# Kernel optimization log

Hardware: AMD Instinct MI355X
Metric: run time of the kernel (lower is better)

The kernel has to match this reference:

```python
import jax, jax.numpy as jnp
import numpy as np
import math

H = 2048          # hidden_size
NH = 16           # num_attn_heads
HD = H // NH      # attn head dim = 128
NFW = 4           # num_lact_heads
FD = H // NFW     # fw head dim = 512
DH = FD           # inter_multi = 1.0
CHUNK = 512       # lact_chunk_size
WINDOW = 2048     # window_size
ROPE_BASE = 500000.0
BASE_LR_INV = math.log(math.expm1(0.001))  # inv_softplus(1e-3)


def rmsnorm(x, w, eps=1e-6):
    return x * jax.lax.rsqrt(jnp.mean(x * x, axis=-1, keepdims=True) + eps) * w


def l2norm(x, eps=1e-12):
    return x * jax.lax.rsqrt(jnp.sum(x * x, axis=-1, keepdims=True) + eps)


def rope(x):  # x: [b, h, s, d], half-split convention
    d = x.shape[-1]
    s = x.shape[2]
    inv = 1.0 / (ROPE_BASE ** (jnp.arange(d // 2, dtype=jnp.float32) / (d // 2)))
    f = jnp.arange(s, dtype=jnp.float32)[:, None] * inv[None, :]  # [s, d/2]
    cos, sin = jnp.cos(f), jnp.sin(f)
    x1, x2 = x[..., : d // 2], x[..., d // 2:]
    return jnp.concatenate([x1 * cos - x2 * sin, x2 * cos + x1 * sin], axis=-1)


def setup_inputs() -> dict:
    key = jax.random.key(0)
    ks = jax.random.split(key, 8)
    b, s = 2, 2048
    return {
        "hidden_states": jax.random.normal(ks[0], (b, s, H), jnp.float32),
        "qkv_w": jax.random.normal(ks[1], (3 * H, H), jnp.float32) / math.sqrt(H),
        "q_norm_w": jnp.ones((H,), jnp.float32),
        "k_norm_w": jnp.ones((H,), jnp.float32),
        "qk_scale": jnp.ones((H, 2), jnp.float32),
        "qk_offset": jnp.zeros((H, 2), jnp.float32),
        "lr_w": jax.random.normal(ks[2], (3 * NFW, H), jnp.float32) / math.sqrt(H),
        "lr_b": jnp.zeros((3 * NFW,), jnp.float32),
        "w0": jax.random.normal(ks[3], (NFW, DH, FD), jnp.float32) / math.sqrt(FD),
        "w1": jax.random.normal(ks[4], (NFW, FD, DH), jnp.float32) / math.sqrt(DH),
        "w2": jax.random.normal(ks[5], (NFW, DH, FD), jnp.float32) / math.sqrt(FD),
        "ttt_norm_w": jnp.ones((FD,), jnp.float32),
        "o_proj_w": jax.random.normal(ks[6], (H, H), jnp.float32) / math.sqrt(H),
    }


def reference(hidden_states, qkv_w, q_norm_w, k_norm_w, qk_scale, qk_offset,
              lr_w, lr_b, w0, w1, w2, ttt_norm_w, o_proj_w):
    x = hidden_states
    b, s, _ = x.shape
    nc = s // CHUNK

    qkv = x @ qkv_w.T
    q, k, v = jnp.split(qkv, 3, axis=-1)
    q = rmsnorm(q, q_norm_w)
    k = rmsnorm(k, k_norm_w)

    # ---- TTT (fast-weight SwiGLU) branch ----
    fq = jax.nn.silu(q * qk_scale[:, 0] + qk_offset[:, 0])
    fk = jax.nn.silu(k * qk_scale[:, 1] + qk_offset[:, 1])
    fv = jax.nn.silu(v)
    tohead = lambda t: t.reshape(b, s, NFW, FD).transpose(0, 2, 1, 3)  # [b,h,s,d]
    fq, fk, fv = l2norm(tohead(fq)), l2norm(tohead(fk)), tohead(fv)

    lr = jax.nn.softplus(x @ lr_w.T + lr_b + BASE_LR_INV)          # [b,s,3*NFW]
    lr = lr.reshape(b, s, 3, NFW).transpose(2, 0, 3, 1)[..., None]  # [3,b,h,s,1]
    lr0, lr1, lr2 = lr[0], lr[1], lr[2]

    chunkify = lambda t: t.reshape(b, NFW, nc, CHUNK, -1).transpose(2, 0, 1, 3, 4)
    qs, ks_, vs = chunkify(fq), chunkify(fk), chunkify(fv)
    l0s, l1s, l2s = chunkify(lr0), chunkify(lr1), chunkify(lr2)

    w0b = jnp.broadcast_to(w0, (b,) + w0.shape)
    w1b = jnp.broadcast_to(w1, (b,) + w1.shape)
    w2b = jnp.broadcast_to(w2, (b,) + w2.shape)

    def step(carry, xs):
        w0c, w1c, w2c = carry
        qc, kc, vc, l0, l1, l2 = xs
        # apply current fast weights to queries (strictly causal across chunks)
        hq = jax.nn.silu(jnp.einsum('bhcd,bhed->bhce', qc, w0c)) * \
             jnp.einsum('bhcd,bhed->bhce', qc, w2c)
        oc = jnp.einsum('bhce,bhde->bhcd', hq, w1c)
        # gradient-descent update on dot-product loss -sum(v * f(k))
        g1 = jnp.einsum('bhcd,bhed->bhce', kc, w0c)
        g2 = jnp.einsum('bhcd,bhed->bhce', kc, w2c)
        gate = jax.nn.silu(g1)
        hidden = gate * g2
        dhidden = jnp.einsum('bhcd,bhde->bhce', vc, w1c)  # w1^T v
        dh2 = dhidden * gate
        sig = jax.nn.sigmoid(g1)
        dh1 = dhidden * g2 * (sig * (1.0 + g1 * (1.0 - sig)))  # silu'(g1)
        w1n = w1c + jnp.einsum('bhcd,bhce->bhde', l1 * vc, hidden)
        w0n = w0c + jnp.einsum('bhce,bhcd->bhed', l0 * dh1, kc)
        w2n = w2c + jnp.einsum('bhce,bhcd->bhed', l2 * dh2, kc)
        return (w0n, w1n, w2n), oc

    _, o_chunks = jax.lax.scan(step, (w0b, w1b, w2b), (qs, ks_, vs, l0s, l1s, l2s))
    o_ttt = o_chunks.transpose(1, 2, 0, 3, 4).reshape(b, NFW, s, FD)
    o_ttt = rmsnorm(o_ttt, ttt_norm_w)
    o_ttt = o_ttt.transpose(0, 2, 1, 3).reshape(b, s, H)

    # ---- sliding-window attention branch ----
    qa = rope(q.reshape(b, s, NH, HD).transpose(0, 2, 1, 3))
    ka = rope(k.reshape(b, s, NH, HD).transpose(0, 2, 1, 3))
    va = v.reshape(b, s, NH, HD).transpose(0, 2, 1, 3)
    scores = jnp.einsum('bhqd,bhkd->bhqk', qa, ka) / math.sqrt(HD)
    i = jnp.arange(s)
    mask = (i[:, None] >= i[None, :]) & (i[:, None] - i[None, :] < WINDOW)
    scores = jnp.where(mask, scores, jnp.float32(-1e9))
    p = jax.nn.softmax(scores, axis=-1)
    attn = jnp.einsum('bhqk,bhkd->bhqd', p, va).transpose(0, 2, 1, 3).reshape(b, s, H)

    return (attn + o_ttt) @ o_proj_w.T
```

## Files before the change

kernel.cpp:

```cpp
#include <hip/hip_runtime.h>
#include <hip/hip_bf16.h>
#include <math.h>

using bf16 = __hip_bfloat16;

namespace {

constexpr int cH = 2048;
constexpr int cNH = 16;
constexpr int cHD = 128;
constexpr int cNFW = 4;
constexpr int cFD = 512;
constexpr int cS = 2048;
constexpr float cRSQRT_HD = 0.08838834764831845f;
constexpr long ZL_ = 262144;
constexpr long ZG_ = 1048576;

typedef __attribute__((ext_vector_type(8))) short short8;
typedef __attribute__((ext_vector_type(4))) float f32x4;

__device__ __forceinline__ float sigmoidf_(float x) { return 1.0f / (1.0f + __expf(-x)); }
__device__ __forceinline__ float b2f(bf16 v) { return __bfloat162float(v); }
__device__ __forceinline__ bf16 f2b(float v) { return __float2bfloat16(v); }
__device__ __forceinline__ unsigned short f2bu(float f) {
  return __builtin_bit_cast(unsigned short, __float2bfloat16(f));
}
__device__ __forceinline__ float bu2f(unsigned u) { return __uint_as_float(u << 16); }

#if defined(__has_builtin)
#if __has_builtin(__builtin_amdgcn_global_load_lds)
#define HAVE_GLOAD 1
#endif
#endif

__device__ __forceinline__ void gload16(const bf16* g, short* ldsbase) {
#ifdef HAVE_GLOAD
  __builtin_amdgcn_global_load_lds((const __attribute__((address_space(1))) void*)g,
                                   (__attribute__((address_space(3))) void*)ldsbase, 16, 0, 0);
#else
  const int l = threadIdx.x & 63;
  *(uint4*)(ldsbase + l * 8) = *(const uint4*)g;
#endif
}

__device__ __forceinline__ void stage16(const bf16* src, short* dst) {
  *(uint4*)dst = *(const uint4*)src;
  *(uint4*)(dst + 8) = *(const uint4*)(src + 8);
}

__device__ __forceinline__ void store1(float* p, float v) { *p = v; }
__device__ __forceinline__ void store1(bf16* p, float v) { *p = f2b(v); }

__device__ __forceinline__ void mm_core32(const bf16* __restrict__ Ab, int lda,
                                          const bf16* __restrict__ Bb, int ldb, int K,
                                          short* As, short* Bs, f32x4 acc[4][4]) {
  const int t = threadIdx.x, lane = t & 63, g = lane >> 4, c16 = lane & 15;
  const int wv = t >> 6, wm = (wv >> 1) * 64, wn = (wv & 1) * 64;
  for (int k0 = 0; k0 < K; k0 += 32) {
    __syncthreads();
    {
      const int ch = wv * 2;
      const bf16* ga = Ab + (size_t)(ch * 16 + (lane >> 2)) * lda + k0 + (lane & 3) * 8;
      gload16(ga, &As[ch * 512]);
      gload16(ga + (size_t)16 * lda, &As[ch * 512 + 512]);
      const bf16* gb = Bb + (size_t)(ch * 16 + (lane >> 2)) * ldb + k0 + (lane & 3) * 8;
      gload16(gb, &Bs[ch * 512]);
      gload16(gb + (size_t)16 * ldb, &Bs[ch * 512 + 512]);
    }
    __syncthreads();
    short8 af[4], bfr[4];
#pragma unroll
    for (int mi = 0; mi < 4; ++mi) af[mi] = *(const short8*)&As[(wm + mi * 16 + c16) * 32 + g * 8];
#pragma unroll
    for (int ni = 0; ni < 4; ++ni) bfr[ni] = *(const short8*)&Bs[(wn + ni * 16 + c16) * 32 + g * 8];
#pragma unroll
    for (int mi = 0; mi < 4; ++mi)
#pragma unroll
      for (int ni = 0; ni < 4; ++ni)
        acc[mi][ni] = __builtin_amdgcn_mfma_f32_16x16x32_bf16(af[mi], bfr[ni], acc[mi][ni], 0, 0, 0);
  }
}

template <bool ACC, bool MIR, typename TC>
__device__ __forceinline__ void mm_store(TC* Cb, bf16* Mb, int ldc, int rb, int cb, f32x4 acc[4][4]) {
  const int t = threadIdx.x, lane = t & 63, g = lane >> 4, c16 = lane & 15;
  const int wv = t >> 6, wm = (wv >> 1) * 64, wn = (wv & 1) * 64;
  const int rbase = rb + wm, cbase = cb + wn;
#pragma unroll
  for (int mi = 0; mi < 4; ++mi)
#pragma unroll
    for (int ni = 0; ni < 4; ++ni) {
      const int col = cbase + ni * 16 + c16;
#pragma unroll
      for (int r = 0; r < 4; ++r) {
        const int row = rbase + mi * 16 + g * 4 + r;
        TC* cp = Cb + (size_t)row * ldc + col;
        if constexpr (ACC) {
          float nv = *cp + acc[mi][ni][r];
          *cp = nv;
          if constexpr (MIR) Mb[(size_t)row * ldc + col] = f2b(nv);
        } else {
          store1(cp, acc[mi][ni][r]);
        }
      }
    }
}

template <typename TC>
__global__ __launch_bounds__(512, 1) void k_mm8(const bf16* __restrict__ A, int lda,
                                                const bf16* __restrict__ B, int ldb,
                                                TC* __restrict__ C, int ldc, int K) {
  __shared__ short LA[3][256 * 64];
  __shared__ short LB[3][128 * 64];
  const int t = threadIdx.x, lane = t & 63, wv = t >> 6;
  const int g = lane >> 4, c16 = lane & 15;
  const int wm = (wv >> 1) * 64, wn = (wv & 1) * 64;
  const bf16* Ab = A + (size_t)blockIdx.y * 256 * lda;
  const bf16* Bb = B + (size_t)blockIdx.x * 128 * ldb;
  const int NKT = K >> 6;
  const int srow = wv * 16 + (lane >> 3);
  const int scol = ((lane & 7) ^ ((lane >> 3) & 7)) * 8;

  auto stA = [&](int buf, int half, int kt) {
    const int ktc = (kt < NKT) ? kt : 0;
    const bf16* src = Ab + (size_t)(half * 128 + srow) * lda + ktc * 64 + scol;
    short* dst = &LA[buf][(half * 128 + wv * 16) * 64];
    gload16(src, dst);
    gload16(src + (size_t)8 * lda, dst + 512);
  };
  auto stB = [&](int buf, int kt) {
    const int ktc = (kt < NKT) ? kt : 0;
    const bf16* src = Bb + (size_t)srow * ldb + ktc * 64 + scol;
    short* dst = &LB[buf][(wv * 16) * 64];
    gload16(src, dst);
    gload16(src + (size_t)8 * ldb, dst + 512);
  };

  f32x4 acc[4][4];
  const f32x4 zero4 = {0.f, 0.f, 0.f, 0.f};
#pragma unroll
  for (int i = 0; i < 4; ++i)
#pragma unroll
    for (int j = 0; j < 4; ++j) acc[i][j] = zero4;

  stA(0, 0, 0); stA(0, 1, 0); stB(0, 0);
  stA(1, 0, 1); stA(1, 1, 1); stB(1, 1);
  asm volatile("s_waitcnt vmcnt(6)" ::: "memory");
  __builtin_amdgcn_s_barrier();

  for (int kt = 0; kt < NKT; ++kt) {
    const int cb = kt % 3, nb = (kt + 2) % 3;
    short8 af[4][2], bfr[4][2];
#pragma unroll
    for (int f = 0; f < 4; ++f)
#pragma unroll
      for (int kk = 0; kk < 2; ++kk) {
        const int ra = wm + f * 16 + c16;
        af[f][kk] = *(const short8*)&LA[cb][ra * 64 + ((kk * 4 + g) ^ (ra & 7)) * 8];
        const int rb_ = wn + f * 16 + c16;
        bfr[f][kk] = *(const short8*)&LB[cb][rb_ * 64 + ((kk * 4 + g) ^ (rb_ & 7)) * 8];
      }
    stA(nb, 0, kt + 2); stA(nb, 1, kt + 2); stB(nb, kt + 2);
    __builtin_amdgcn_s_setprio(1);
#pragma unroll
    for (int f = 0; f < 4; ++f)
#pragma unroll
      for (int ni = 0; ni < 4; ++ni)
#pragma unroll
        for (int kk = 0; kk < 2; ++kk)
          acc[f][ni] = __builtin_amdgcn_mfma_f32_16x16x32_bf16(
              af[f][kk], bfr[ni][kk], acc[f][ni], 0, 0, 0);
    __builtin_amdgcn_s_setprio(0);
    asm volatile("s_waitcnt vmcnt(6)" ::: "memory");
    __builtin_amdgcn_s_barrier();
  }

  const int rbase = blockIdx.y * 256 + wm, cbase = blockIdx.x * 128 + wn;
#pragma unroll
  for (int fr = 0; fr < 4; ++fr)
#pragma unroll
    for (int ni = 0; ni < 4; ++ni) {
      const int col = cbase + ni * 16 + c16;
#pragma unroll
      for (int r = 0; r < 4; ++r)
        store1(C + (size_t)(rbase + fr * 16 + g * 4 + r) * ldc + col, acc[fr][ni][r]);
    }
}

__global__ __launch_bounds__(256) void k_fuse1(const bf16* __restrict__ fq, const bf16* __restrict__ fk,
                                               const bf16* __restrict__ fv,
                                               const bf16* __restrict__ w0b, const bf16* __restrict__ w1t,
                                               const bf16* __restrict__ w2b,
                                               bf16* __restrict__ hq, bf16* __restrict__ trH,
                                               bf16* __restrict__ trD1, bf16* __restrict__ trD2,
                                               bf16* __restrict__ trK, bf16* __restrict__ trV,
                                               const float* __restrict__ lr0, const float* __restrict__ lr1,
                                               const float* __restrict__ lr2,
                                               const bf16* __restrict__ occ,
                                               const float* __restrict__ tw, bf16* __restrict__ y,
                                               int chunk) {
  __shared__ short S[12288];
  __shared__ float red[4];
  const int id = blockIdx.x, t = threadIdx.x;
  const size_t choff = (size_t)chunk * 262144;

  if (id < 512) {
    const int bh = id >> 6, tile = id & 63, by = tile >> 3, bx = tile & 7;
    const int lane = t & 63, g = lane >> 4, c16 = lane & 15, wv = t >> 6;
    const int wm = (wv >> 1) * 32, wn = (wv & 1) * 32;
    const bf16* Aq = fq + (size_t)bh * ZG_ + choff + (size_t)(by * 64) * cFD;
    const bf16* Ak = fk + (size_t)bh * ZG_ + choff + (size_t)(by * 64) * cFD;
    const bf16* Av = fv + (size_t)bh * ZG_ + choff + (size_t)(by * 64) * cFD;
    const bf16* B0 = w0b + (size_t)bh * ZL_ + (size_t)(bx * 64) * cFD;
    const bf16* B2 = w2b + (size_t)bh * ZL_ + (size_t)(bx * 64) * cFD;
    const bf16* B1 = w1t + (size_t)bh * ZL_ + (size_t)(bx * 64) * cFD;

    f32x4 acc[5][2][2];
    const f32x4 zero4 = {0.f, 0.f, 0.f, 0.f};
#pragma unroll
    for (int v = 0; v < 5; ++v)
#pragma unroll
      for (int i = 0; i < 2; ++i)
#pragma unroll
        for (int j = 0; j < 2; ++j) acc[v][i][j] = zero4;

    const int srow = wv * 16 + (lane >> 2), scol = (lane & 3) * 8;
    for (int k0 = 0; k0 < 512; k0 += 32) {
      __syncthreads();
      gload16(Aq + (size_t)srow * cFD + k0 + scol, &S[0 + wv * 512]);
      gload16(Ak + (size_t)srow * cFD + k0 + scol, &S[2048 + wv * 512]);
      gload16(Av + (size_t)srow * cFD + k0 + scol, &S[4096 + wv * 512]);
      gload16(B0 + (size_t)srow * cFD + k0 + scol, &S[6144 + wv * 512]);
      gload16(B2 + (size_t)srow * cFD + k0 + scol, &S[8192 + wv * 512]);
      gload16(B1 + (size_t)srow * cFD + k0 + scol, &S[10240 + wv * 512]);
      __syncthreads();
      short8 aq[2], ak[2], av[2], b0[2], b2[2], b1[2];
#pragma unroll
      for (int mi = 0; mi < 2; ++mi) {
        const int ro = (wm + mi * 16 + c16) * 32 + g * 8;
        aq[mi] = *(const short8*)&S[0 + ro];
        ak[mi] = *(const short8*)&S[2048 + ro];
        av[mi] = *(const short8*)&S[4096 + ro];
      }
#pragma unroll
      for (int ni = 0; ni < 2; ++ni) {
        const int ro = (wn + ni * 16 + c16) * 32 + g * 8;
        b0[ni] = *(const short8*)&S[6144 + ro];
        b2[ni] = *(const short8*)&S[8192 + ro];
        b1[ni] = *(const short8*)&S[10240 + ro];
      }
#pragma unroll
      for (int mi = 0; mi < 2; ++mi)
#pragma unroll
        for (int ni = 0; ni < 2; ++ni) {
          acc[0][mi][ni] = __builtin_amdgcn_mfma_f32_16x16x32_bf16(aq[mi], b0[ni], acc[0][mi][ni], 0, 0, 0);
          acc[1][mi][ni] = __builtin_amdgcn_mfma_f32_16x16x32_bf16(aq[mi], b2[ni], acc[1][mi][ni], 0, 0, 0);
          acc[2][mi][ni] = __builtin_amdgcn_mfma_f32_16x16x32_bf16(ak[mi], b0[ni], acc[2][mi][ni], 0, 0, 0);
          acc[3][mi][ni] = __builtin_amdgcn_mfma_f32_16x16x32_bf16(ak[mi], b2[ni], acc[3][mi][ni], 0, 0, 0);
          acc[4][mi][ni] = __builtin_amdgcn_mfma_f32_16x16x32_bf16(av[mi], b1[ni], acc[4][mi][ni], 0, 0, 0);
        }
    }

    float l0v[2][4], l2v[2][4];
#pragma unroll
    for (int mi = 0; mi < 2; ++mi)
#pragma unroll
      for (int r = 0; r < 4; ++r) {
        const int row = by * 64 + wm + mi * 16 + g * 4 + r;
        l0v[mi][r] = lr0[bh * 2048 + chunk * 512 + row];
        l2v[mi][r] = lr2[bh * 2048 + chunk * 512 + row];
      }
#pragma unroll
    for (int mi = 0; mi < 2; ++mi)
#pragma unroll
      for (int ni = 0; ni < 2; ++ni)
#pragma unroll
        for (int r = 0; r < 4; ++r) {
          float hq1 = acc[0][mi][ni][r], hq2 = acc[1][mi][ni][r];
          float g1 = acc[2][mi][ni][r], g2 = acc[3][mi][ni][r], dh = acc[4][mi][ni][r];
          acc[0][mi][ni][r] = hq1 * sigmoidf_(hq1) * hq2;
          float sg = sigmoidf_(g1);
          float gate = g1 * sg;
          acc[1][mi][ni][r] = gate * g2;
          acc[2][mi][ni][r] = l0v[mi][r] * dh * g2 * (sg * (1.0f + g1 * (1.0f - sg)));
          acc[3][mi][ni][r] = l2v[mi][r] * dh * gate;
        }

    short* Ts = S;
    bf16* dst0 = hq + (size_t)bh * ZL_;
    bf16* dstT[3] = {trH + (size_t)bh * ZL_, trD1 + (size_t)bh * ZL_, trD2 + (size_t)bh * ZL_};
#pragma unroll
    for (int rd = 0; rd < 4; ++rd) {
      __syncthreads();
#pragma unroll
      for (int mi = 0; mi < 2; ++mi)
#pragma unroll
        for (int ni = 0; ni < 2; ++ni)
#pragma unroll
          for (int r = 0; r < 4; ++r) {
            const int row = wm + mi * 16 + g * 4 + r, col = wn + ni * 16 + c16;
            if (rd == 0) Ts[row * 66 + col] = (short)f2bu(acc[0][mi][ni][r]);
            else Ts[col * 66 + row] = (short)f2bu(acc[rd][mi][ni][r]);
          }
      __syncthreads();
      const int rr = t >> 2, cs = (t & 3) * 16;
      unsigned short u[16] __attribute__((aligned(16)));
#pragma unroll
      for (int i = 0; i < 16; ++i) u[i] = (unsigned short)Ts[rr * 66 + cs + i];
      bf16* dp = (rd == 0) ? (dst0 + (size_t)(by * 64 + rr) * cFD + bx * 64 + cs)
                           : (dstT[rd - 1] + (size_t)(bx * 64 + rr) * cFD + by * 64 + cs);
      *(uint4*)dp = *(uint4*)u;
      *(uint4*)(dp + 8) = *(uint4*)(u + 8);
    }
  } else if (id < 1536) {
    short* Ts = S;
    const int id2 = id - 512;
    const int var = id2 >> 9, bh = (id2 >> 6) & 7, by = (id2 >> 3) & 7, bx = id2 & 7;
    const bf16* src = ((var == 0) ? fk : fv) + choff + (size_t)bh * ZG_;
    bf16* dst = ((var == 0) ? trK : trV) + (size_t)bh * ZL_;
    {
      const int rr = t >> 2, cseg = (t & 3) * 16;
      if (var == 0) {
        stage16(src + (size_t)(by * 64 + rr) * cFD + bx * 64 + cseg, &Ts[rr * 72 + cseg]);
      } else {
        const float s = lr1[bh * 2048 + chunk * 512 + by * 64 + rr];
        const bf16* p = src + (size_t)(by * 64 + rr) * cFD + bx * 64 + cseg;
        unsigned short u[16] __attribute__((aligned(16)));
#pragma unroll
        for (int i = 0; i < 16; ++i) u[i] = f2bu(b2f(p[i]) * s);
        *(uint4*)&Ts[rr * 72 + cseg] = *(uint4*)u;
        *(uint4*)&Ts[rr * 72 + cseg + 8] = *(uint4*)(u + 8);
      }
    }
    __syncthreads();
    {
      const int oc_ = t >> 2, rseg = (t & 3) * 16;
      unsigned short u[16] __attribute__((aligned(16)));
#pragma unroll
      for (int i = 0; i < 16; ++i) u[i] = (unsigned short)Ts[(rseg + i) * 72 + oc_];
      bf16* dp = dst + (size_t)(bx * 64 + oc_) * cFD + by * 64 + rseg;
      *(uint4*)dp = *(uint4*)u;
      *(uint4*)(dp + 8) = *(uint4*)(u + 8);
    }
  } else {
    const int rrow = id - 1536;
    const int bh = rrow >> 9, rr = rrow & 511;
    const bf16* src = occ + ((size_t)bh * 512 + rr) * 512;
    float v0 = b2f(src[t]), v1 = b2f(src[t + 256]);
    float ss = v0 * v0 + v1 * v1;
    for (int d = 32; d; d >>= 1) ss += __shfl_down(ss, d);
    if ((t & 63) == 0) red[t >> 6] = ss;
    __syncthreads();
    const float rstd = rsqrtf((red[0] + red[1] + red[2] + red[3]) / cFD + 1e-6f);
    const int si = (chunk - 1) * 512 + rr;
    bf16* dst = y + ((size_t)((bh >> 2) * cS) + si) * cH + (bh & 3) * cFD;
    dst[t] = f2b(b2f(dst[t]) + v0 * rstd * tw[t]);
    dst[t + 256] = f2b(b2f(dst[t + 256]) + v1 * rstd * tw[t + 256]);
  }
}

__global__ __launch_bounds__(256) void k_updna(const bf16* __restrict__ trV, const bf16* __restrict__ trH,
                                               const bf16* __restrict__ trD1, const bf16* __restrict__ trD2,
                                               const bf16* __restrict__ trK,
                                               const bf16* __restrict__ hq, const bf16* __restrict__ w1bc,
                                               float* w0s, float* w1s, float* w2s,
                                               bf16* w0b, bf16* w1bn, bf16* w2b, bf16* w1t,
                                               bf16* __restrict__ occ) {
  __shared__ short Sh[8704];
  const int id = blockIdx.x, t = threadIdx.x;
  const int lane = t & 63, g = lane >> 4, c16 = lane & 15, wv = t >> 6;
  if (id < 384) {
    short* As = Sh;
    short* Bs = Sh + 4096;
    const int z = id >> 4, tile = id & 15, by = tile >> 2, bx = tile & 3;
    const int var = z >> 3, bh = z & 7;
    const bf16 *Aa, *Bb;
    if (var == 0) {
      Aa = trV + (size_t)bh * ZL_ + (size_t)by * 128 * cFD;
      Bb = trH + (size_t)bh * ZL_ + (size_t)bx * 128 * cFD;
    } else if (var == 1) {
      Aa = trD1 + (size_t)bh * ZL_ + (size_t)by * 128 * cFD;
      Bb = trK + (size_t)bh * ZL_ + (size_t)bx * 128 * cFD;
    } else {
      Aa = trD2 + (size_t)bh * ZL_ + (size_t)by * 128 * cFD;
      Bb = trK + (size_t)bh * ZL_ + (size_t)bx * 128 * cFD;
    }
    f32x4 acc[4][4];
    const f32x4 zero4 = {0.f, 0.f, 0.f, 0.f};
#pragma unroll
    for (int i = 0; i < 4; ++i)
#pragma unroll
      for (int j = 0; j < 4; ++j) acc[i][j] = zero4;
    mm_core32(Aa, cFD, Bb, cFD, cFD, As, Bs, acc);
    if (var == 1) {
      mm_store<true, true>(w0s + (size_t)bh * ZL_, w0b + (size_t)bh * ZL_, cFD, by * 128, bx * 128, acc);
    } else if (var == 2) {
      mm_store<true, true>(w2s + (size_t)bh * ZL_, w2b + (size_t)bh * ZL_, cFD, by * 128, bx * 128, acc);
    } else {
      float* W = w1s + (size_t)bh * ZL_;
      bf16* M = w1bn + (size_t)bh * ZL_;
      const int wm = (wv >> 1) * 64, wn = (wv & 1) * 64;
#pragma unroll
      for (int mi = 0; mi < 4; ++mi)
#pragma unroll
        for (int ni = 0; ni < 4; ++ni) {
          const int col = bx * 128 + wn + ni * 16 + c16;
#pragma unroll
          for (int r = 0; r < 4; ++r) {
            const int row = by * 128 + wm + mi * 16 + g * 4 + r;
            float nv = W[(size_t)row * cFD + col] + acc[mi][ni][r];
            W[(size_t)row * cFD + col] = nv;
            M[(size_t)row * cFD + col] = f2b(nv);
            acc[mi][ni][r] = nv;
          }
        }
      bf16* T = w1t + (size_t)bh * ZL_;
      short* Ts = Sh;
#pragma unroll
      for (int rd = 0; rd < 2; ++rd) {
        __syncthreads();
        if (wn == rd * 64) {
#pragma unroll
          for (int mi = 0; mi < 4; ++mi)
#pragma unroll
            for (int ni = 0; ni < 4; ++ni) {
              const int cc = ni * 16 + c16;
              unsigned short u[4] __attribute__((aligned(8)));
#pragma unroll
              for (int r = 0; r < 4; ++r) u[r] = f2bu(acc[mi][ni][r]);
              *(uint2*)&Ts[cc * 136 + wm + mi * 16 + g * 4] = *(uint2*)u;
            }
        }
        __syncthreads();
        const int cc = t >> 2, seg = (t & 3) * 32;
        unsigned short u[32] __attribute__((aligned(16)));
#pragma unroll
        for (int i = 0; i < 32; ++i) u[i] = (unsigned short)Ts[cc * 136 + seg + i];
        bf16* dp = T + (size_t)(bx * 128 + rd * 64 + cc) * cFD + by * 128 + seg;
        *(uint4*)dp = *(uint4*)u;
        *(uint4*)(dp + 8) = *(uint4*)(u + 8);
        *(uint4*)(dp + 16) = *(uint4*)(u + 16);
        *(uint4*)(dp + 24) = *(uint4*)(u + 24);
      }
    }
  } else {
    short* As = Sh;
    short* Bs = Sh + 4096;
    const int id2 = id - 384;
    const int bh = id2 >> 4, tile = id2 & 15, by = tile >> 2, bx = tile & 3;
    const bf16* Aa = hq + (size_t)bh * ZL_ + (size_t)by * 128 * cFD;
    const bf16* Bb = w1bc + (size_t)bh * ZL_ + (size_t)bx * 128 * cFD;
    f32x4 acc[4][4];
    const f32x4 zero4 = {0.f, 0.f, 0.f, 0.f};
#pragma unroll
    for (int i = 0; i < 4; ++i)
#pragma unroll
      for (int j = 0; j < 4; ++j) acc[i][j] = zero4;
    mm_core32(Aa, cFD, Bb, cFD, cFD, As, Bs, acc);
    mm_store<false, false>(occ + (size_t)bh * ZL_, (bf16*)nullptr, cFD, by * 128, bx * 128, acc);
  }
}

__global__ __launch_bounds__(256) void k_normcvt(const bf16* __restrict__ occ,
                                                 const float* __restrict__ tw, bf16* __restrict__ y,
                                                 const float* __restrict__ opw, bf16* __restrict__ opwb,
                                                 int chunk) {
  __shared__ float red[4];
  const int id = blockIdx.x, t = threadIdx.x;
  if (id < 4096) {
    const int bh = id >> 9, rr = id & 511;
    const bf16* src = occ + ((size_t)bh * 512 + rr) * 512;
    float v0 = b2f(src[t]), v1 = b2f(src[t + 256]);
    float ss = v0 * v0 + v1 * v1;
    for (int d = 32; d; d >>= 1) ss += __shfl_down(ss, d);
    if ((t & 63) == 0) red[t >> 6] = ss;
    __syncthreads();
    const float rstd = rsqrtf((red[0] + red[1] + red[2] + red[3]) / cFD + 1e-6f);
    const int si = chunk * 512 + rr;
    bf16* dst = y + ((size_t)((bh >> 2) * cS) + si) * cH + (bh & 3) * cFD;
    dst[t] = f2b(b2f(dst[t]) + v0 * rstd * tw[t]);
    dst[t + 256] = f2b(b2f(dst[t + 256]) + v1 * rstd * tw[t + 256]);
  } else {
    const size_t i = ((size_t)(id - 4096) * 256 + t) * 8;
    float4 a = *(const float4*)(opw + i), b = *(const float4*)(opw + i + 4);
    unsigned short u[8] __attribute__((aligned(16)));
    u[0] = f2bu(a.x); u[1] = f2bu(a.y); u[2] = f2bu(a.z); u[3] = f2bu(a.w);
    u[4] = f2bu(b.x); u[5] = f2bu(b.y); u[6] = f2bu(b.z); u[7] = f2bu(b.w);
    *(uint4*)(opwb + i) = *(uint4*)u;
  }
}

__global__ __launch_bounds__(256) void k_prep(const float* __restrict__ x, const float* __restrict__ qkv_w,
                                              const float* __restrict__ w0, const float* __restrict__ w1,
                                              const float* __restrict__ w2,
                                              const float* __restrict__ lr_w, const float* __restrict__ lr_b,
                                              bf16* __restrict__ xb, bf16* __restrict__ qkvwb,
                                              float* __restrict__ w0s, float* __restrict__ w1s,
                                              float* __restrict__ w2s,
                                              float* __restrict__ ct, float* __restrict__ stb,
                                              float* lr0, float* lr1, float* lr2, float base) {
  __shared__ float xbuf[cH];
  const int id = blockIdx.x, t = threadIdx.x;
  if (id < 4096) {
    const size_t i = ((size_t)id * 256 + t) * 8;
    float4 a = *(const float4*)(x + i), b = *(const float4*)(x + i + 4);
    unsigned short u[8] __attribute__((aligned(16)));
    u[0] = f2bu(a.x); u[1] = f2bu(a.y); u[2] = f2bu(a.z); u[3] = f2bu(a.w);
    u[4] = f2bu(b.x); u[5] = f2bu(b.y); u[6] = f2bu(b.z); u[7] = f2bu(b.w);
    *(uint4*)(xb + i) = *(uint4*)u;
  } else if (id < 10240) {
    const size_t i = ((size_t)(id - 4096) * 256 + t) * 8;
    float4 a = *(const float4*)(qkv_w + i), b = *(const float4*)(qkv_w + i + 4);
    unsigned short u[8] __attribute__((aligned(16)));
    u[0] = f2bu(a.x); u[1] = f2bu(a.y); u[2] = f2bu(a.z); u[3] = f2bu(a.w);
    u[4] = f2bu(b.x); u[5] = f2bu(b.y); u[6] = f2bu(b.z); u[7] = f2bu(b.w);
    *(uint4*)(qkvwb + i) = *(uint4*)u;
  } else if (id < 16384) {
    const int sub = id - 10240;
    const int w = sub >> 11, blk = sub & 2047;
    const size_t i = ((size_t)blk * 256 + t) * 4;
    const int f = (int)((i >> 18) & 3);
    const size_t off = i & 262143;
    const float* src = (w == 0) ? w0 : (w == 1) ? w1 : w2;
    float* dst = (w == 0) ? w0s : (w == 1) ? w1s : w2s;
    *(float4*)(dst + i) = *(const float4*)(src + (size_t)f * 262144 + off);
  } else if (id < 16896) {
    const int gid = (id - 16384) * 256 + t;
    const int si = gid >> 6, jj = gid & 63;
    float inv = powf(500000.0f, -(float)jj / 64.0f);
    float ang = (float)si * inv;
    ct[(size_t)si * 64 + jj] = cosf(ang);
    stb[(size_t)si * 64 + jj] = sinf(ang);
  } else {
    const int token = id - 16896, b_ = token >> 11, si = token & 2047;
    const int wv = t >> 6, lane = t & 63;
    const float* xr = x + (size_t)token * cH;
    for (int i = t; i < cH; i += 256) xbuf[i] = xr[i];
    __syncthreads();
#pragma unroll
    for (int jj = 0; jj < 3; ++jj) {
      const int j = wv * 3 + jj;
      const float* wr = lr_w + (size_t)j * cH;
      float s = 0.f;
      for (int k = lane; k < cH; k += 64) s += xbuf[k] * wr[k];
      for (int d = 32; d; d >>= 1) s += __shfl_down(s, d);
      if (lane == 0) {
        float v = s + lr_b[j] + base;
        float sp = (v > 15.f) ? v : log1pf(expf(v));
        const int tt = j >> 2, f = j & 3;
        float* dst = (tt == 0 ? lr0 : tt == 1 ? lr1 : lr2);
        dst[(size_t)(b_ * cNFW + f) * cS + si] = sp;
      }
    }
  }
}

__global__ __launch_bounds__(256) void k_post2(bf16* __restrict__ qkvh,
                                               const float* __restrict__ qnw, const float* __restrict__ knw,
                                               const float* __restrict__ ct, const float* __restrict__ stb,
                                               bf16* __restrict__ qa, bf16* __restrict__ ka,
                                               bf16* __restrict__ vt) {
  __shared__ short smem[8704];
  __shared__ float red[4];
  const int id = blockIdx.x, t = threadIdx.x;
  if (id < 4096) {
    float* buf = (float*)smem;
    const int token = id, b_ = token >> 11, si = token & 2047;
    bf16* base = qkvh + (size_t)token * 3 * cH;
    for (int pass = 0; pass < 2; ++pass) {
      __syncthreads();
      bf16* src = base + pass * cH;
      const float* nw = pass ? knw : qnw;
      float ss = 0.f;
      for (int i = t; i < cH; i += 256) {
        float v = b2f(src[i]);
        buf[i] = v;
        ss += v * v;
      }
      for (int d = 32; d; d >>= 1) ss += __shfl_down(ss, d);
      if ((t & 63) == 0) red[t >> 6] = ss;
      __syncthreads();
      const float rstd = rsqrtf((red[0] + red[1] + red[2] + red[3]) / cH + 1e-6f);
      for (int i = t; i < cH; i += 256) {
        float v = buf[i] * rstd * nw[i];
        buf[i] = v;
        src[i] = f2b(v);
      }
      __syncthreads();
      bf16* dst = pass ? ka : qa;
      const float scale = pass ? 1.f : cRSQRT_HD;
      const int hh = t >> 4, j0 = (t & 15) * 4;
      const float* cr = ct + (size_t)si * 64 + j0;
      const float* sr = stb + (size_t)si * 64 + j0;
      bf16* drow = dst + ((size_t)(b_ * cNH + hh) * cS + si) * cHD;
      unsigned short u1[4] __attribute__((aligned(8))), u2[4] __attribute__((aligned(8)));
#pragma unroll
      for (int i = 0; i < 4; ++i) {
        float x1 = buf[hh * cHD + j0 + i], x2 = buf[hh * cHD + 64 + j0 + i];
        u1[i] = f2bu((x1 * cr[i] - x2 * sr[i]) * scale);
        u2[i] = f2bu((x2 * cr[i] + x1 * sr[i]) * scale);
      }
      *(uint2*)(drow + j0) = *(uint2*)u1;
      *(uint2*)(drow + 64 + j0) = *(uint2*)u2;
    }
  } else {
    short* Ts = smem;
    const int id2 = id - 4096;
    const int tile = id2 & 31, h = (id2 >> 5) & 15, b_ = id2 >> 9;
    {
      const int r = t >> 2, seg = (t & 3) * 32;
      const bf16* src = qkvh + ((size_t)(b_ * cS) + tile * 64 + r) * 3 * cH + 2 * cH + h * cHD + seg;
      stage16(src, &Ts[r * 136 + seg]);
      stage16(src + 16, &Ts[r * 136 + seg + 16]);
    }
    __syncthreads();
    {
      const int d = t >> 1, seg2 = (t & 1) * 32;
      unsigned short u[32] __attribute__((aligned(16)));
#pragma unroll
      for (int i = 0; i < 32; ++i) u[i] = (unsigned short)Ts[(seg2 + i) * 136 + d];
      bf16* dp = vt + ((size_t)(b_ * cNH + h) * cHD + d) * cS + tile * 64 + seg2;
      *(uint4*)dp = *(uint4*)u;
      *(uint4*)(dp + 8) = *(uint4*)(u + 8);
      *(uint4*)(dp + 16) = *(uint4*)(u + 16);
      *(uint4*)(dp + 24) = *(uint4*)(u + 24);
    }
  }
}

__global__ __launch_bounds__(256) void k_mid(const bf16* __restrict__ qkvh,
                                             const float* __restrict__ qk_scale,
                                             const float* __restrict__ qk_offset,
                                             bf16* fq, bf16* fk, bf16* fv,
                                             const float* __restrict__ w0s_, bf16* __restrict__ w0b_,
                                             const float* __restrict__ w1s_, bf16* __restrict__ w1t_) {
  __shared__ short Ts[64 * 72];
  const int id = blockIdx.x, t = threadIdx.x;
  if (id < 4096) {
    const int token = id, b_ = token >> 11, si = token & 2047;
    const bf16* base = qkvh + (size_t)token * 3 * cH;
#pragma unroll
    for (int pass = 0; pass < 2; ++pass) {
      const bf16* src = base + pass * cH;
      bf16* fdst = pass ? fk : fq;
      const int head = t >> 6, lane = t & 63;
      float f[8];
      float ss2 = 0.f;
#pragma unroll
      for (int k = 0; k < 8; ++k) {
        const int idx = head * cFD + lane + k * 64;
        float v = b2f(src[idx]);
        float u = v * qk_scale[idx * 2 + pass] + qk_offset[idx * 2 + pass];
        float fv_ = u * sigmoidf_(u);
        f[k] = fv_;
        ss2 += fv_ * fv_;
      }
      for (int d = 1; d < 64; d <<= 1) ss2 += __shfl_xor(ss2, d);
      const float sc2 = rsqrtf(ss2 + 1e-12f);
      bf16* dst = fdst + ((size_t)(b_ * cNFW + head) * cS + si) * cFD;
#pragma unroll
      for (int k = 0; k < 8; ++k) dst[lane + k * 64] = f2b(f[k] * sc2);
    }
    const bf16* vr = base + 2 * cH;
    for (int i = t; i < cH; i += 256) {
      float v = b2f(vr[i]);
      fv[((size_t)(b_ * cNFW + (i >> 9)) * cS + si) * cFD + (i & 511)] = f2b(v * sigmoidf_(v));
    }
  } else if (id < 7168) {
    const size_t i = ((size_t)(id - 4096) * 256 + t) * 8;
    float4 a = *(const float4*)(w0s_ + i), b = *(const float4*)(w0s_ + i + 4);
    unsigned short u[8] __attribute__((aligned(16)));
    u[0] = f2bu(a.x); u[1] = f2bu(a.y); u[2] = f2bu(a.z); u[3] = f2bu(a.w);
    u[4] = f2bu(b.x); u[5] = f2bu(b.y); u[6] = f2bu(b.z); u[7] = f2bu(b.w);
    *(uint4*)(w0b_ + i) = *(uint4*)u;
  } else {
    const int id3 = id - 7168;
    const int bh = id3 >> 6, tile = id3 & 63, by = tile >> 3, bx = tile & 7;
    {
      const int rr = t >> 2, cseg = (t & 3) * 16;
      const float* p = w1s_ + (size_t)bh * ZL_ + (size_t)(by * 64 + rr) * cFD + bx * 64 + cseg;
      unsigned short u[16] __attribute__((aligned(16)));
#pragma unroll
      for (int i = 0; i < 16; ++i) u[i] = f2bu(p[i]);
      *(uint4*)&Ts[rr * 72 + cseg] = *(uint4*)u;
      *(uint4*)&Ts[rr * 72 + cseg + 8] = *(uint4*)(u + 8);
    }
    __syncthreads();
    {
      const int oc_ = t >> 2, rseg = (t & 3) * 16;
      unsigned short u[16] __attribute__((aligned(16)));
#pragma unroll
      for (int i = 0; i < 16; ++i) u[i] = (unsigned short)Ts[(rseg + i) * 72 + oc_];
      bf16* dp = w1t_ + (size_t)bh * ZL_ + (size_t)(bx * 64 + oc_) * cFD + by * 64 + rseg;
      *(uint4*)dp = *(uint4*)u;
      *(uint4*)(dp + 8) = *(uint4*)(u + 8);
    }
  }
}

__global__ __launch_bounds__(512) void k_attn6(const bf16* __restrict__ qa, const bf16* __restrict__ ka,
                                               const bf16* __restrict__ vt, bf16* __restrict__ y) {
  const int id = blockIdx.x;
  const int xcd = id & 7;
  const int j = id >> 3;
  const int p = j & 7;
  const int hb = (j >> 3) * 8 + xcd;
  const int h = hb & 15, b_ = hb >> 4;
  __shared__ short KsP[9216];
  __shared__ short Vts[128 * 72];
  const int t = threadIdx.x, lane = t & 63, g = lane >> 4, c16 = lane & 15, wv = t >> 6;
  const size_t hbq = (size_t)(b_ * cNH + h) * cS;
  const bf16* vb = vt + (size_t)(b_ * cNH + h) * (size_t)(cHD * cS);
  const int r = t >> 3, seg = (t & 7) * 16;
  const int dv = t >> 2, seg2 = (t & 3) * 16;
  const f32x4 zero4 = {0.f, 0.f, 0.f, 0.f};

  for (int half = 0; half < 2; ++half) {
    const int qt = half ? p : 15 - p;
    const int q0 = qt * 128;
    const int nkt = 2 * qt + 2;
    short8 qf[4];
    {
      const bf16* qsrc = qa + (hbq + q0 + wv * 16 + c16) * cHD;
#pragma unroll
      for (int ks = 0; ks < 4; ++ks) qf[ks] = *(const short8*)(qsrc + ks * 32 + g * 8);
    }
    f32x4 o[8];
#pragma unroll
    for (int i = 0; i < 8; ++i) o[i] = zero4;
    float m[4], l[4];
#pragma unroll
    for (int rr = 0; rr < 4; ++rr) { m[rr] = -1e30f; l[rr] = 0.f; }

    uint4 kp0, kp1, vp0, vp1;
    {
      const bf16* ksrc = ka + (hbq + r) * cHD + seg;
      kp0 = *(const uint4*)ksrc; kp1 = *(const uint4*)(ksrc + 8);
      const bf16* vsrc = vb + (size_t)dv * cS + seg2;
      vp0 = *(const uint4*)vsrc; vp1 = *(const uint4*)(vsrc + 8);
    }

    for (int kt = 0; kt < nkt; ++kt) {
      __syncthreads();
      {
        short* kd = &KsP[r * 136 + seg];
        *(uint4*)kd = kp0; *(uint4*)(kd + 8) = kp1;
        short* vd = &Vts[dv * 72 + seg2];
        *(uint4*)vd = vp0; *(uint4*)(vd + 8) = vp1;
      }
      __syncthreads();
      if (kt + 1 < nkt) {
        const bf16* ksrc = ka + (hbq + (kt + 1) * 64 + r) * cHD + seg;
        kp0 = *(const uint4*)ksrc; kp1 = *(const uint4*)(ksrc + 8);
        const bf16* vsrc = vb + (size_t)dv * cS + (kt + 1) * 64 + seg2;
        vp0 = *(const uint4*)vsrc; vp1 = *(const uint4*)(vsrc + 8);
      } else if (half == 0) {
        const bf16* ksrc = ka + (hbq + r) * cHD + seg;
        kp0 = *(const uint4*)ksrc; kp1 = *(const uint4*)(ksrc + 8);
        const bf16* vsrc = vb + (size_t)dv * cS + seg2;
        vp0 = *(const uint4*)vsrc; vp1 = *(const uint4*)(vsrc + 8);
      }
// ... 179 lines not shown
```

Baseline: 660.8 us.

## Load GEMM A operand directly into registers, bypassing LDS staging

In the k_mm8 GEMM, the A tile is no longer staged through a triple-buffered LDS array. Each wave now reads its A fragments straight from global memory into registers, using an even/odd register double buffer. The main loop is unrolled by two so it can alternate between the two buffers. B keeps its LDS triple buffer. This drops the LDS traffic and footprint for A, but waves that share rows now fetch the same A data twice. The strided 16-byte per-lane global loads may also coalesce poorly, and the loop assumes an even K-tile count.

```diff
diff --git a/kernel.cpp b/kernel.cpp
--- a/kernel.cpp
+++ b/kernel.cpp
@@ -110,7 +110,6 @@
 __global__ __launch_bounds__(512, 1) void k_mm8(const bf16* __restrict__ A, int lda,
                                                 const bf16* __restrict__ B, int ldb,
                                                 TC* __restrict__ C, int ldc, int K) {
-  __shared__ short LA[3][256 * 64];
   __shared__ short LB[3][128 * 64];
   const int t = threadIdx.x, lane = t & 63, wv = t >> 6;
   const int g = lane >> 4, c16 = lane & 15;
@@ -121,13 +120,6 @@
   const int srow = wv * 16 + (lane >> 3);
   const int scol = ((lane & 7) ^ ((lane >> 3) & 7)) * 8;
 
-  auto stA = [&](int buf, int half, int kt) {
-    const int ktc = (kt < NKT) ? kt : 0;
-    const bf16* src = Ab + (size_t)(half * 128 + srow) * lda + ktc * 64 + scol;
-    short* dst = &LA[buf][(half * 128 + wv * 16) * 64];
-    gload16(src, dst);
-    gload16(src + (size_t)8 * lda, dst + 512);
-  };
   auto stB = [&](int buf, int kt) {
     const int ktc = (kt < NKT) ? kt : 0;
     const bf16* src = Bb + (size_t)srow * ldb + ktc * 64 + scol;
@@ -135,6 +127,15 @@
     gload16(src, dst);
     gload16(src + (size_t)8 * ldb, dst + 512);
   };
+  auto loadA = [&](short8 dst[4][2], int kt) {
+    const int ktc = (kt < NKT) ? kt : 0;
+#pragma unroll
+    for (int f = 0; f < 4; ++f)
+#pragma unroll
+      for (int kk = 0; kk < 2; ++kk)
+        dst[f][kk] = *(const short8*)(Ab + (size_t)(wm + f * 16 + c16) * lda +
+                                      ktc * 64 + kk * 32 + g * 8);
+  };
 
   f32x4 acc[4][4];
   const f32x4 zero4 = {0.f, 0.f, 0.f, 0.f};
@@ -143,36 +144,70 @@
 #pragma unroll
     for (int j = 0; j < 4; ++j) acc[i][j] = zero4;
 
-  stA(0, 0, 0); stA(0, 1, 0); stB(0, 0);
-  stA(1, 0, 1); stA(1, 1, 1); stB(1, 1);
-  asm volatile("s_waitcnt vmcnt(6)" ::: "memory");
+  short8 afE[4][2], afO[4][2];
+
+  stB(0, 0);
+  stB(1, 1);
+  loadA(afE, 0);
+  asm volatile("s_waitcnt vmcnt(0)" ::: "memory");
   __builtin_amdgcn_s_barrier();
 
-  for (int kt = 0; kt < NKT; ++kt) {
-    const int cb = kt % 3, nb = (kt + 2) % 3;
-    short8 af[4][2], bfr[4][2];
-#pragma unroll
-    for (int f = 0; f < 4; ++f)
-#pragma unroll
-      for (int kk = 0; kk < 2; ++kk) {
-        const int ra = wm + f * 16 + c16;
-        af[f][kk] = *(const short8*)&LA[cb][ra * 64 + ((kk * 4 + g) ^ (ra & 7)) * 8];
-        const int rb_ = wn + f * 16 + c16;
-        bfr[f][kk] = *(const short8*)&LB[cb][rb_ * 64 + ((kk * 4 + g) ^ (rb_ & 7)) * 8];
-      }
-    stA(nb, 0, kt + 2); stA(nb, 1, kt + 2); stB(nb, kt + 2);
-    __builtin_amdgcn_s_setprio(1);
-#pragma unroll
-    for (int f = 0; f < 4; ++f)
+  int rb = 0;
+  for (int it = 0; it < NKT; it += 2) {
+    {
+      const int kt = it;
+      const int sb = (rb >= 1) ? rb - 1 : 2;
+      loadA(afO, kt + 1);
+      stB(sb, kt + 2);
+      short8 bfr[4][2];
 #pragma unroll
       for (int ni = 0; ni < 4; ++ni)
 #pragma unroll
-        for (int kk = 0; kk < 2; ++kk)
-          acc[f][ni] = __builtin_amdgcn_mfma_f32_16x16x32_bf16(
-              af[f][kk], bfr[ni][kk], acc[f][ni], 0, 0, 0);
-    __builtin_amdgcn_s_setprio(0);
-    asm volatile("s_waitcnt vmcnt(6)" ::: "memory");
-    __builtin_amdgcn_s_barrier();
+        for (int kk = 0; kk < 2; ++kk) {
+          const int rr = wn + ni * 16 + c16;
+          bfr[ni][kk] = *(const short8*)&LB[rb][rr * 64 + ((kk * 4 + g) ^ (rr & 7)) * 8];
+        }
+      __builtin_amdgcn_s_setprio(1);
+#pragma unroll
+      for (int f = 0; f < 4; ++f)
+#pragma unroll
+        for (int ni = 0; ni < 4; ++ni)
+#pragma unroll
+          for (int kk = 0; kk < 2; ++kk)
+            acc[f][ni] = __builtin_amdgcn_mfma_f32_16x16x32_bf16(
+                afE[f][kk], bfr[ni][kk], acc[f][ni], 0, 0, 0);
+      __builtin_amdgcn_s_setprio(0);
+      asm volatile("s_waitcnt vmcnt(4)" ::: "memory");
+      __builtin_amdgcn_s_barrier();
+      rb = (rb + 1 < 3) ? rb + 1 : 0;
+    }
+    {
+      const int kt = it + 1;
+      const int sb = (rb >= 1) ? rb - 1 : 2;
+      loadA(afE, kt + 1);
+      stB(sb, kt + 2);
+      short8 bfr[4][2];
+#pragma unroll
+      for (int ni = 0; ni < 4; ++ni)
+#pragma unroll
+        for (int kk = 0; kk < 2; ++kk) {
+          const int rr = wn + ni * 16 + c16;
+          bfr[ni][kk] = *(const short8*)&LB[rb][rr * 64 + ((kk * 4 + g) ^ (rr & 7)) * 8];
+        }
+      __builtin_amdgcn_s_setprio(1);
+#pragma unroll
+      for (int f = 0; f < 4; ++f)
+#pragma unroll
+        for (int ni = 0; ni < 4; ++ni)
+#pragma unroll
+          for (int kk = 0; kk < 2; ++kk)
+            acc[f][ni] = __builtin_amdgcn_mfma_f32_16x16x32_bf16(
+                afO[f][kk], bfr[ni][kk], acc[f][ni], 0, 0, 0);
+      __builtin_amdgcn_s_setprio(0);
+      asm volatile("s_waitcnt vmcnt(4)" ::: "memory");
+      __builtin_amdgcn_s_barrier();
+      rb = (rb + 1 < 3) ? rb + 1 : 0;
+    }
   }
 
   const int rbase = blockIdx.y * 256 + wm, cbase = blockIdx.x * 128 + wn;
```

Result: slower. 819.1 us (+24.0%).

## Triple-buffer LDS staging with XOR swizzle in TTT chunk GEMM kernels

Applied to the files above, without the earlier changes.

Replaces the single-buffered load-sync-compute loops in the per-chunk fused GEMM and weight-update kernels with a 3-stage LDS ring that prefetches two K-tiles ahead, using vmcnt waits and raw barriers instead of two __syncthreads per step. LDS rows get an XOR column swizzle to reduce bank conflicts, and MFMA sections are wrapped in s_setprio. This is meant to hide global-load latency behind matrix math, at the cost of tripling LDS use, which may lower occupancy. It also issues redundant clamped loads on the last iterations.

```diff
diff --git a/kernel.cpp b/kernel.cpp
--- a/kernel.cpp
+++ b/kernel.cpp
@@ -51,33 +51,51 @@
 __device__ __forceinline__ void store1(float* p, float v) { *p = v; }
 __device__ __forceinline__ void store1(bf16* p, float v) { *p = f2b(v); }
 
-__device__ __forceinline__ void mm_core32(const bf16* __restrict__ Ab, int lda,
-                                          const bf16* __restrict__ Bb, int ldb, int K,
-                                          short* As, short* Bs, f32x4 acc[4][4]) {
+__device__ __forceinline__ void mm_core32p(const bf16* __restrict__ Ab, int lda,
+                                           const bf16* __restrict__ Bb, int ldb, int K,
+                                           short* As, short* Bs, f32x4 acc[4][4]) {
   const int t = threadIdx.x, lane = t & 63, g = lane >> 4, c16 = lane & 15;
   const int wv = t >> 6, wm = (wv >> 1) * 64, wn = (wv & 1) * 64;
-  for (int k0 = 0; k0 < K; k0 += 32) {
-    __syncthreads();
-    {
-      const int ch = wv * 2;
-      const bf16* ga = Ab + (size_t)(ch * 16 + (lane >> 2)) * lda + k0 + (lane & 3) * 8;
-      gload16(ga, &As[ch * 512]);
-      gload16(ga + (size_t)16 * lda, &As[ch * 512 + 512]);
-      const bf16* gb = Bb + (size_t)(ch * 16 + (lane >> 2)) * ldb + k0 + (lane & 3) * 8;
-      gload16(gb, &Bs[ch * 512]);
-      gload16(gb + (size_t)16 * ldb, &Bs[ch * 512 + 512]);
-    }
-    __syncthreads();
+  const int NKT = K >> 5;
+  const int scolp = ((lane & 3) ^ ((lane >> 2) & 3)) * 8;
+
+  auto stg = [&](int buf, int kt) {
+    const int ktc = (kt < NKT) ? kt : 0;
+    const bf16* ga = Ab + (size_t)(wv * 32 + (lane >> 2)) * lda + ktc * 32 + scolp;
+    short* da = &As[buf * 4096 + (wv * 32) * 32];
+    gload16(ga, da);
+    gload16(ga + (size_t)16 * lda, da + 512);
+    const bf16* gb = Bb + (size_t)(wv * 32 + (lane >> 2)) * ldb + ktc * 32 + scolp;
+    short* db = &Bs[buf * 4096 + (wv * 32) * 32];
+    gload16(gb, db);
+    gload16(gb + (size_t)16 * ldb, db + 512);
+  };
+
+  stg(0, 0);
+  stg(1, 1);
+  asm volatile("s_waitcnt vmcnt(4)" ::: "memory");
+  __builtin_amdgcn_s_barrier();
+
+  for (int kt = 0; kt < NKT; ++kt) {
+    const int cb = kt % 3, nb = (kt + 2) % 3;
     short8 af[4], bfr[4];
 #pragma unroll
-    for (int mi = 0; mi < 4; ++mi) af[mi] = *(const short8*)&As[(wm + mi * 16 + c16) * 32 + g * 8];
-#pragma unroll
-    for (int ni = 0; ni < 4; ++ni) bfr[ni] = *(const short8*)&Bs[(wn + ni * 16 + c16) * 32 + g * 8];
+    for (int mi = 0; mi < 4; ++mi) {
+      const int ra = wm + mi * 16 + c16;
+      af[mi] = *(const short8*)&As[cb * 4096 + ra * 32 + (g ^ (ra & 3)) * 8];
+      const int rbn = wn + mi * 16 + c16;
+      bfr[mi] = *(const short8*)&Bs[cb * 4096 + rbn * 32 + (g ^ (rbn & 3)) * 8];
+    }
+    stg(nb, kt + 2);
+    __builtin_amdgcn_s_setprio(1);
 #pragma unroll
     for (int mi = 0; mi < 4; ++mi)
 #pragma unroll
       for (int ni = 0; ni < 4; ++ni)
         acc[mi][ni] = __builtin_amdgcn_mfma_f32_16x16x32_bf16(af[mi], bfr[ni], acc[mi][ni], 0, 0, 0);
+    __builtin_amdgcn_s_setprio(0);
+    asm volatile("s_waitcnt vmcnt(4)" ::: "memory");
+    __builtin_amdgcn_s_barrier();
   }
 }
 
@@ -199,7 +217,7 @@
                                                const bf16* __restrict__ occ,
                                                const float* __restrict__ tw, bf16* __restrict__ y,
                                                int chunk) {
-  __shared__ short S[12288];
+  __shared__ short S[36864];
   __shared__ float red[4];
   const int id = blockIdx.x, t = threadIdx.x;
   const size_t choff = (size_t)chunk * 262144;
@@ -224,31 +242,44 @@
 #pragma unroll
         for (int j = 0; j < 2; ++j) acc[v][i][j] = zero4;
 
-    const int srow = wv * 16 + (lane >> 2), scol = (lane & 3) * 8;
-    for (int k0 = 0; k0 < 512; k0 += 32) {
-      __syncthreads();
-      gload16(Aq + (size_t)srow * cFD + k0 + scol, &S[0 + wv * 512]);
-      gload16(Ak + (size_t)srow * cFD + k0 + scol, &S[2048 + wv * 512]);
-      gload16(Av + (size_t)srow * cFD + k0 + scol, &S[4096 + wv * 512]);
-      gload16(B0 + (size_t)srow * cFD + k0 + scol, &S[6144 + wv * 512]);
-      gload16(B2 + (size_t)srow * cFD + k0 + scol, &S[8192 + wv * 512]);
-      gload16(B1 + (size_t)srow * cFD + k0 + scol, &S[10240 + wv * 512]);
-      __syncthreads();
+    const int srowp = wv * 16 + (lane >> 2);
+    const int scolp = ((lane & 3) ^ ((lane >> 2) & 3)) * 8;
+    auto stg1 = [&](int op, const bf16* base, int buf, int ktc) {
+      gload16(base + (size_t)srowp * cFD + ktc * 32 + scolp,
+              &S[(op * 3 + buf) * 2048 + (wv * 16) * 32]);
+    };
+    auto stg6 = [&](int buf, int kt) {
+      const int ktc = (kt < 16) ? kt : 0;
+      stg1(0, Aq, buf, ktc); stg1(1, Ak, buf, ktc); stg1(2, Av, buf, ktc);
+      stg1(3, B0, buf, ktc); stg1(4, B2, buf, ktc); stg1(5, B1, buf, ktc);
+    };
+
+    stg6(0, 0);
+    stg6(1, 1);
+    asm volatile("s_waitcnt vmcnt(6)" ::: "memory");
+    __builtin_amdgcn_s_barrier();
+
+    for (int kt = 0; kt < 16; ++kt) {
+      const int cb = kt % 3, nb = (kt + 2) % 3;
       short8 aq[2], ak[2], av[2], b0[2], b2[2], b1[2];
 #pragma unroll
       for (int mi = 0; mi < 2; ++mi) {
-        const int ro = (wm + mi * 16 + c16) * 32 + g * 8;
-        aq[mi] = *(const short8*)&S[0 + ro];
-        ak[mi] = *(const short8*)&S[2048 + ro];
-        av[mi] = *(const short8*)&S[4096 + ro];
+        const int ra = wm + mi * 16 + c16;
+        const int ro = ra * 32 + (g ^ (ra & 3)) * 8;
+        aq[mi] = *(const short8*)&S[(0 * 3 + cb) * 2048 + ro];
+        ak[mi] = *(const short8*)&S[(1 * 3 + cb) * 2048 + ro];
+        av[mi] = *(const short8*)&S[(2 * 3 + cb) * 2048 + ro];
       }
 #pragma unroll
       for (int ni = 0; ni < 2; ++ni) {
-        const int ro = (wn + ni * 16 + c16) * 32 + g * 8;
-        b0[ni] = *(const short8*)&S[6144 + ro];
-        b2[ni] = *(const short8*)&S[8192 + ro];
-        b1[ni] = *(const short8*)&S[10240 + ro];
-      }
+        const int rbn = wn + ni * 16 + c16;
+        const int ro = rbn * 32 + (g ^ (rbn & 3)) * 8;
+        b0[ni] = *(const short8*)&S[(3 * 3 + cb) * 2048 + ro];
+        b2[ni] = *(const short8*)&S[(4 * 3 + cb) * 2048 + ro];
+        b1[ni] = *(const short8*)&S[(5 * 3 + cb) * 2048 + ro];
+      }
+      stg6(nb, kt + 2);
+      __builtin_amdgcn_s_setprio(1);
 #pragma unroll
       for (int mi = 0; mi < 2; ++mi)
 #pragma unroll
@@ -259,6 +290,9 @@
           acc[3][mi][ni] = __builtin_amdgcn_mfma_f32_16x16x32_bf16(ak[mi], b2[ni], acc[3][mi][ni], 0, 0, 0);
           acc[4][mi][ni] = __builtin_amdgcn_mfma_f32_16x16x32_bf16(av[mi], b1[ni], acc[4][mi][ni], 0, 0, 0);
         }
+      __builtin_amdgcn_s_setprio(0);
+      asm volatile("s_waitcnt vmcnt(6)" ::: "memory");
+      __builtin_amdgcn_s_barrier();
     }
 
     float l0v[2][4], l2v[2][4];
@@ -366,12 +400,12 @@
                                                float* w0s, float* w1s, float* w2s,
                                                bf16* w0b, bf16* w1bn, bf16* w2b, bf16* w1t,
                                                bf16* __restrict__ occ) {
-  __shared__ short Sh[8704];
+  __shared__ short Sh[24576];
   const int id = blockIdx.x, t = threadIdx.x;
   const int lane = t & 63, g = lane >> 4, c16 = lane & 15, wv = t >> 6;
   if (id < 384) {
     short* As = Sh;
-    short* Bs = Sh + 4096;
+    short* Bs = Sh + 12288;
     const int z = id >> 4, tile = id & 15, by = tile >> 2, bx = tile & 3;
     const int var = z >> 3, bh = z & 7;
     const bf16 *Aa, *Bb;
@@ -391,7 +425,7 @@
     for (int i = 0; i < 4; ++i)
 #pragma unroll
       for (int j = 0; j < 4; ++j) acc[i][j] = zero4;
-    mm_core32(Aa, cFD, Bb, cFD, cFD, As, Bs, acc);
+    mm_core32p(Aa, cFD, Bb, cFD, cFD, As, Bs, acc);
     if (var == 1) {
       mm_store<true, true>(w0s + (size_t)bh * ZL_, w0b + (size_t)bh * ZL_, cFD, by * 128, bx * 128, acc);
     } else if (var == 2) {
@@ -445,7 +479,7 @@
     }
   } else {
     short* As = Sh;
-    short* Bs = Sh + 4096;
+    short* Bs = Sh + 12288;
     const int id2 = id - 384;
     const int bh = id2 >> 4, tile = id2 & 15, by = tile >> 2, bx = tile & 3;
     const bf16* Aa = hq + (size_t)bh * ZL_ + (size_t)by * 128 * cFD;
@@ -456,7 +490,7 @@
     for (int i = 0; i < 4; ++i)
 #pragma unroll
       for (int j = 0; j < 4; ++j) acc[i][j] = zero4;
-    mm_core32(Aa, cFD, Bb, cFD, cFD, As, Bs, acc);
+    mm_core32p(Aa, cFD, Bb, cFD, cFD, As, Bs, acc);
     mm_store<false, false>(occ + (size_t)bh * ZL_, (bf16*)nullptr, cFD, by * 128, bx * 128, acc);
   }
 }
```

Measured after the change: 670.2 us. No clear change (+1.4%).
